# Kernel optimization log

Hardware: AMD Instinct MI355X
Metric: run time of the kernel (lower is better)

Reference implementation:

```python
import jax, jax.numpy as jnp
import numpy as np

B, N, E, H = 1, 4096, 2048, 16
D = E // H  # head_size = 128
DEGREE = 4
LN_EPS = 1e-5
ROPE_BASE = 10000.0


def rope_cos_sin(n, d):
    # [n, d//2] tables
    inv_freq = 1.0 / (ROPE_BASE ** (jnp.arange(0, d, 2, dtype=jnp.float32) / d))
    t = jnp.arange(n, dtype=jnp.float32)[:, None] * inv_freq[None, :]
    return jnp.cos(t), jnp.sin(t)


def apply_rope(x, cos, sin):
    # x: [b, n, h, d]; rotate-half RoPE
    x1, x2 = jnp.split(x, 2, axis=-1)
    c = cos[None, :, None, :]
    s = sin[None, :, None, :]
    return jnp.concatenate([x1 * c - x2 * s, x1 * s + x2 * c], axis=-1)


def layernorm(x, scale, bias, eps=LN_EPS):
    m = jnp.mean(x, axis=-1, keepdims=True)
    v = jnp.var(x, axis=-1, keepdims=True)
    return (x - m) * jax.lax.rsqrt(v + eps) * scale + bias


def polynomial_attention(q, k, v, degree, is_causal):
    # q,k,v: [b, h, n, d]
    a = jnp.einsum('bhnd,bhmd->bhnm', q, k) ** degree
    if is_causal:
        a = jnp.tril(a)
    denom = jnp.sum(a, axis=-1, keepdims=True)
    return jnp.einsum('bhnm,bhmd->bhnd', a / denom, v)


def setup_inputs() -> dict:
    key = jax.random.key(0)
    k0, k1, k2 = jax.random.split(key, 3)
    x = jax.random.normal(k0, (B, N, E), dtype=jnp.float32)
    # Dense(3*emb_dim, use_bias=False) and Dense(emb_dim, use_bias=False)
    w_qkv = jax.random.normal(k1, (E, 3 * E), dtype=jnp.float32) * (1.0 / np.sqrt(E))
    w_out = jax.random.normal(k2, (E, E), dtype=jnp.float32) * (1.0 / np.sqrt(E))
    # shared pre-attention LayerNorm over head dim (flax init: scale=1, bias=0)
    ln_scale = jnp.ones((D,), dtype=jnp.float32)
    ln_bias = jnp.zeros((D,), dtype=jnp.float32)
    return {"x": x, "w_qkv": w_qkv, "w_out": w_out,
            "ln_scale": ln_scale, "ln_bias": ln_bias}


def reference(x, w_qkv, w_out, ln_scale, ln_bias):
    b, n, e = x.shape
    proj = x @ w_qkv                              # [b, n, 3e]
    q, k, v = jnp.split(proj, 3, axis=-1)
    q = q.reshape(b, n, H, D)
    k = k.reshape(b, n, H, D)
    v = v.reshape(b, n, H, D)
    cos, sin = rope_cos_sin(n, D)
    q = apply_rope(q, cos, sin)
    k = apply_rope(k, cos, sin)
    # transpose branch (non-softmax): [b, h, n, d]
    q = q.transpose(0, 2, 1, 3)
    k = k.transpose(0, 2, 1, 3)
    v = v.transpose(0, 2, 1, 3)
    # shared pre_attn LayerNorm applied to q and k
    q = layernorm(q, ln_scale, ln_bias)
    k = layernorm(k, ln_scale, ln_bias)
    out = polynomial_attention(q, k, v, DEGREE, True)  # [b, h, n, d]
    out = out.transpose(0, 2, 1, 3).reshape(b, n, e)
    out = out @ w_out                              # dropout rate 0 / inference: identity
    return out
```

## Files before the change

### kernel.cpp

```cpp
#include <hip/hip_runtime.h>
#include <stdint.h>
#include <math.h>

#define N_SEQ 4096
#define EDIM  2048
#define NH    16
#define HD    128

typedef __attribute__((ext_vector_type(8))) short bf16x8;
typedef __attribute__((ext_vector_type(4))) float f32x4;

#define AS1 __attribute__((address_space(1)))
#define AS3 __attribute__((address_space(3)))

__device__ __forceinline__ void gll16(const unsigned short* g, unsigned short* l) {
    __builtin_amdgcn_global_load_lds((const AS1 unsigned int*)g,
                                     (AS3 unsigned int*)l, 16, 0, 0);
}

__device__ __forceinline__ unsigned short f2bf(float f) {
    union { float f; unsigned u; } v; v.f = f;
    unsigned r = v.u + 0x7FFFu + ((v.u >> 16) & 1u);
    return (unsigned short)(r >> 16);
}
__device__ __forceinline__ float bf2f(unsigned short h) {
    union { unsigned u; float f; } v; v.u = ((unsigned)h) << 16;
    return v.f;
}

__global__ void k_convert_x(const float* __restrict__ x,
                            unsigned short* __restrict__ xb, int n4) {
    int i = blockIdx.x * blockDim.x + threadIdx.x;
    int stride = gridDim.x * blockDim.x;
    for (; i < n4; i += stride) {
        float4 v = ((const float4*)x)[i];
        ushort4 o;
        o.x = f2bf(v.x); o.y = f2bf(v.y); o.z = f2bf(v.z); o.w = f2bf(v.w);
        ((ushort4*)xb)[i] = o;
    }
}

__global__ void k_transpose_f32_bf16(const float* __restrict__ in,
                                     unsigned short* __restrict__ out,
                                     int R, int C) {
    __shared__ unsigned short Ls[64][68];
    const int c0 = blockIdx.x * 64, r0 = blockIdx.y * 64;
    const int t = threadIdx.x;
    #pragma unroll
    for (int i = 0; i < 4; ++i) {
        int ch = i * 256 + t;
        int r = ch >> 4, c4 = (ch & 15) * 4;
        float4 v = *(const float4*)&in[(size_t)(r0 + r) * C + c0 + c4];
        ushort4 o;
        o.x = f2bf(v.x); o.y = f2bf(v.y); o.z = f2bf(v.z); o.w = f2bf(v.w);
        *(ushort4*)&Ls[r][c4] = o;
    }
    __syncthreads();
    #pragma unroll
    for (int i = 0; i < 2; ++i) {
        int ch = i * 256 + t;
        int rr = ch >> 3, c8 = (ch & 7) * 8;
        unsigned short vals[8];
        #pragma unroll
        for (int j = 0; j < 8; ++j) vals[j] = Ls[c8 + j][rr];
        uint4 pk;
        pk.x = (unsigned)vals[0] | ((unsigned)vals[1] << 16);
        pk.y = (unsigned)vals[2] | ((unsigned)vals[3] << 16);
        pk.z = (unsigned)vals[4] | ((unsigned)vals[5] << 16);
        pk.w = (unsigned)vals[6] | ((unsigned)vals[7] << 16);
        *(uint4*)&out[(size_t)(c0 + rr) * R + r0 + c8] = pk;
    }
}

template<int F32OUT>
__launch_bounds__(256, 2)
__global__ void k_gemm_bt(const unsigned short* __restrict__ A,
                          const unsigned short* __restrict__ Bt,
                          void* __restrict__ C,
                          int M, int N, int K) {
    __shared__ unsigned short sh[2 * 128 * 64];
    unsigned short* As = sh;
    unsigned short* Bs = sh + 128 * 64;

    const int t = threadIdx.x;
    const int wave = t >> 6, lane = t & 63;
    const int wm = wave >> 1, wn = wave & 1;
    const int lg = lane >> 4, lr = lane & 15;

    const int nbx = gridDim.x;
    const int nwg = nbx * gridDim.y;
    int bid = blockIdx.y * nbx + blockIdx.x;
    int swz = (bid & 7) * (nwg >> 3) + (bid >> 3);
    const int m0 = (swz / nbx) * 128;
    const int n0 = (swz % nbx) * 128;

    const unsigned short* aptr = A  + (size_t)m0 * K;
    const unsigned short* bptr = Bt + (size_t)n0 * K;

    f32x4 acc[4][4];
    #pragma unroll
    for (int i = 0; i < 4; ++i)
        #pragma unroll
        for (int j = 0; j < 4; ++j) acc[i][j] = f32x4{0.f, 0.f, 0.f, 0.f};

    int schr[4], srow[4], scb[4];
    #pragma unroll
    for (int i = 0; i < 4; ++i) {
        int ch = (i * 4 + wave) * 64 + lane;
        schr[i] = ch;
        srow[i] = ch >> 3;
        scb[i]  = (ch & 7) ^ ((ch >> 3) & 7);
    }

    const int nkb = K >> 6;
    for (int kb = 0; kb < nkb; ++kb) {
        __syncthreads();
        #pragma unroll
        for (int i = 0; i < 4; ++i) {
            const size_t goff = (size_t)srow[i] * K + (size_t)kb * 64 + scb[i] * 8;
            gll16(&aptr[goff], &As[schr[i] * 8]);
            gll16(&bptr[goff], &Bs[schr[i] * 8]);
        }
        __syncthreads();

        #pragma unroll
        for (int kk = 0; kk < 2; ++kk) {
            bf16x8 af[4], bf[4];
            const int cbx = ((kk * 4 + lg) ^ (lr & 7)) * 8;
            #pragma unroll
            for (int i = 0; i < 4; ++i) {
                af[i] = *(const bf16x8*)&As[(wm * 64 + i * 16 + lr) * 64 + cbx];
                bf[i] = *(const bf16x8*)&Bs[(wn * 64 + i * 16 + lr) * 64 + cbx];
            }
            #pragma unroll
            for (int i = 0; i < 4; ++i)
                #pragma unroll
                for (int j = 0; j < 4; ++j)
                    acc[i][j] = __builtin_amdgcn_mfma_f32_16x16x32_bf16(af[i], bf[j], acc[i][j], 0, 0, 0);
        }
    }

    if (F32OUT) {
        #pragma unroll
        for (int i = 0; i < 4; ++i) {
            int row0 = m0 + wm * 64 + i * 16 + lg * 4;
            #pragma unroll
            for (int j = 0; j < 4; ++j) {
                int col = n0 + wn * 64 + j * 16 + lr;
                #pragma unroll
                for (int r = 0; r < 4; ++r)
                    ((float*)C)[(size_t)(row0 + r) * N + col] = acc[i][j][r];
            }
        }
    } else {
        __syncthreads();
        unsigned short* Cs = sh;
        #pragma unroll
        for (int i = 0; i < 4; ++i) {
            #pragma unroll
            for (int j = 0; j < 4; ++j) {
                int col = wn * 64 + j * 16 + lr;
                #pragma unroll
                for (int r = 0; r < 4; ++r)
                    Cs[(wm * 64 + i * 16 + lg * 4 + r) * 128 + col] = f2bf(acc[i][j][r]);
            }
        }
        __syncthreads();
        #pragma unroll
        for (int i = 0; i < 8; ++i) {
            int ch = i * 256 + t;
            int row = ch >> 4, c8 = (ch & 15) * 8;
            *(uint4*)&((unsigned short*)C)[(size_t)(m0 + row) * N + n0 + c8] =
                *(const uint4*)&Cs[row * 128 + c8];
        }
    }
}

__global__ void k_ropeln(const unsigned short* __restrict__ proj,
                         const float* __restrict__ ln_scale,
                         const float* __restrict__ ln_bias,
                         unsigned short* __restrict__ Qh,
                         unsigned short* __restrict__ Kh) {
    const int n = blockIdx.x;
    const int wave = threadIdx.x >> 6, lane = threadIdx.x & 63;
    float inv = expf(-((float)(2 * lane) / 128.0f) * 9.210340371976184f);
    float ang = (float)n * inv;
    float c = cosf(ang), s = sinf(ang);
    const float sc1 = ln_scale[lane], sc2 = ln_scale[lane + 64];
    const float b1 = ln_bias[lane],  b2 = ln_bias[lane + 64];

    for (int r = wave; r < 32; r += 4) {
        int h = r >> 1, qk = r & 1;
        const unsigned short* src = proj + (size_t)n * (3 * EDIM) + qk * EDIM + h * HD;
        float x1 = bf2f(src[lane]), x2 = bf2f(src[lane + 64]);
        float o1 = x1 * c - x2 * s;
        float o2 = x1 * s + x2 * c;
        float sum = o1 + o2, sq = o1 * o1 + o2 * o2;
        #pragma unroll
        for (int d = 1; d < 64; d <<= 1) {
            sum += __shfl_xor(sum, d);
            sq  += __shfl_xor(sq, d);
        }
        float mean = sum * (1.0f / 128.0f);
        float var = sq * (1.0f / 128.0f) - mean * mean;
        float rstd = rsqrtf(var + 1e-5f);
        float y1 = (o1 - mean) * rstd * sc1 + b1;
        float y2 = (o2 - mean) * rstd * sc2 + b2;
        unsigned short* dst = (qk ? Kh : Qh) + ((size_t)h * N_SEQ + n) * HD;
        dst[lane]      = f2bf(y1);
        dst[lane + 64] = f2bf(y2);
    }
}

__global__ void k_vtrans(const unsigned short* __restrict__ proj,
                         unsigned short* __restrict__ Vt) {
    __shared__ unsigned short Ls[64][136];
    const int h = blockIdx.y;
    const int n0 = blockIdx.x * 64;
    const int t = threadIdx.x;
    #pragma unroll
    for (int i = 0; i < 4; ++i) {
        int ch = i * 256 + t;
        int r = ch >> 4, d0 = (ch & 15) * 8;
        uint4 v = *(const uint4*)&proj[(size_t)(n0 + r) * (3 * EDIM) + 2 * EDIM + h * HD + d0];
        *(uint4*)&Ls[r][d0] = v;
    }
    __syncthreads();
    #pragma unroll
    for (int i = 0; i < 4; ++i) {
        int ch = i * 256 + t;
        int d = ch >> 3, p = ch & 7;
        unsigned short vals[8];
        #pragma unroll
        for (int j = 0; j < 8; ++j) {
            int ko = 32 * (p >> 2) + 16 * (j >> 2) + 4 * (p & 3) + (j & 3);
            vals[j] = Ls[ko][d];
        }
        uint4 pk;
        pk.x = (unsigned)vals[0] | ((unsigned)vals[1] << 16);
        pk.y = (unsigned)vals[2] | ((unsigned)vals[3] << 16);
        pk.z = (unsigned)vals[4] | ((unsigned)vals[5] << 16);
        pk.w = (unsigned)vals[6] | ((unsigned)vals[7] << 16);
        *(uint4*)&Vt[((size_t)h * HD + d) * N_SEQ + n0 + p * 8] = pk;
    }
}

__launch_bounds__(256, 2)
__global__ void k_attn(const unsigned short* __restrict__ Qh,
                       const unsigned short* __restrict__ Kh,
                       const unsigned short* __restrict__ Vt,
                       unsigned short* __restrict__ O) {
    __shared__ unsigned short pool[4 * 8192];

    const int t = threadIdx.x;
    const int w = t >> 6, lane = t & 63;
    const int lg = lane >> 4, lr = lane & 15;

    const int s = blockIdx.x & 255;
    const int batch = blockIdx.x >> 8;
    const int x = s & 7;
    const int hb = (s >> 3) & 1;
    const int h = x * 2 + hb;
    const int qq = s >> 4;
    const int qb = batch ? qq : (31 - qq);
    const int q0 = qb * 128;
    const int qbase = q0 + w * 32;

    bf16x8 qf[2][4];
    #pragma unroll
    for (int mi = 0; mi < 2; ++mi)
        #pragma unroll
        for (int kk = 0; kk < 4; ++kk)
            qf[mi][kk] = *(const bf16x8*)&Qh[((size_t)h * N_SEQ + qbase + mi * 16 + lr) * HD + kk * 32 + lg * 8];

    f32x4 acc[2][8];
    #pragma unroll
    for (int i = 0; i < 2; ++i)
        #pragma unroll
        for (int j = 0; j < 8; ++j) acc[i][j] = f32x4{0.f, 0.f, 0.f, 0.f};
    f32x4 accd[2];
    accd[0] = f32x4{0.f, 0.f, 0.f, 0.f};
    accd[1] = f32x4{0.f, 0.f, 0.f, 0.f};

    bf16x8 onesf;
    {
        short ov = (lr == 0) ? (short)0x3F80 : (short)0;
        #pragma unroll
        for (int j = 0; j < 8; ++j) onesf[j] = ov;
    }

    int kch[4], vch[4];
    const unsigned short* kg[4];
    const unsigned short* vg[4];
    #pragma unroll
    for (int i = 0; i < 4; ++i) {
        int ch = i * 256 + t;
        kch[i] = ch;
        int r = ch >> 4, p = ch & 15;
        int csrc = (p & 8) | ((p ^ r) & 7);
        kg[i] = Kh + ((size_t)h * N_SEQ + r) * HD + csrc * 8;
    }
    #pragma unroll
    for (int i = 0; i < 4; ++i) {
        int ch = i * 256 + t;
        vch[i] = ch;
        int d = ch >> 3, p2 = ch & 7;
        int c2src = (p2 ^ d) & 7;
        vg[i] = Vt + ((size_t)h * HD + d) * N_SEQ + c2src * 8;
    }

    const int nkb = 2 * qb + 2;

    union U8 { unsigned u[4]; bf16x8 v; };

    auto stage = [&](unsigned short* Kn, unsigned short* Vn) {
        #pragma unroll
        for (int i = 0; i < 4; ++i) { gll16(kg[i], Kn + kch[i] * 8); kg[i] += 64 * HD; }
        #pragma unroll
        for (int i = 0; i < 4; ++i) { gll16(vg[i], Vn + vch[i] * 8); vg[i] += 64; }
    };

    auto compute = [&](int k0, const unsigned short* Kc, const unsigned short* Vc) {
        f32x4 sa[2][4];
        #pragma unroll
        for (int i = 0; i < 2; ++i)
            #pragma unroll
            for (int j = 0; j < 4; ++j) sa[i][j] = f32x4{0.f, 0.f, 0.f, 0.f};
        #pragma unroll
        for (int nn = 0; nn < 2; ++nn) {
            bf16x8 kf[2][4];
            #pragma unroll
            for (int nj = 0; nj < 2; ++nj)
                #pragma unroll
                for (int kk = 0; kk < 4; ++kk) {
                    int row = (nn * 2 + nj) * 16 + lr;
                    int c = kk * 4 + lg;
                    int cs = (c & 8) | ((c ^ row) & 7);
                    kf[nj][kk] = *(const bf16x8*)&Kc[row * 128 + cs * 8];
                }
            __builtin_amdgcn_s_setprio(1);
            #pragma unroll
            for (int kk = 0; kk < 4; ++kk)
                #pragma unroll
                for (int nj = 0; nj < 2; ++nj)
                    #pragma unroll
                    for (int mi = 0; mi < 2; ++mi)
                        sa[mi][nn * 2 + nj] = __builtin_amdgcn_mfma_f32_16x16x32_bf16(
                            kf[nj][kk], qf[mi][kk], sa[mi][nn * 2 + nj], 0, 0, 0);
            __builtin_amdgcn_s_setprio(0);
        }

        unsigned wreg[2][4][2];
        const bool nomask = (k0 + 63 <= qbase);
        #pragma unroll
        for (int mi = 0; mi < 2; ++mi)
            #pragma unroll
            for (int nj = 0; nj < 4; ++nj) {
                float p[4];
                #pragma unroll
                for (int r = 0; r < 4; ++r) {
                    float sv = sa[mi][nj][r];
                    float t2 = sv * sv;
                    p[r] = t2 * t2;
                    if (!nomask) {
                        int gk = k0 + nj * 16 + lg * 4 + r;
                        int gq = qbase + mi * 16 + lr;
                        p[r] = (gk <= gq) ? p[r] : 0.0f;
                    }
                }
                asm("v_cvt_pk_bf16_f32 %0, %1, %2" : "=v"(wreg[mi][nj][0]) : "v"(p[0]), "v"(p[1]));
                asm("v_cvt_pk_bf16_f32 %0, %1, %2" : "=v"(wreg[mi][nj][1]) : "v"(p[2]), "v"(p[3]));
            }

        #pragma unroll
        for (int s2 = 0; s2 < 2; ++s2) {
            bf16x8 pa[2];
            #pragma unroll
            for (int mi = 0; mi < 2; ++mi) {
                U8 u;
                u.u[0] = wreg[mi][2 * s2][0];
                u.u[1] = wreg[mi][2 * s2][1];
                u.u[2] = wreg[mi][2 * s2 + 1][0];
                u.u[3] = wreg[mi][2 * s2 + 1][1];
                pa[mi] = u.v;
            }
            __builtin_amdgcn_s_setprio(1);
            #pragma unroll
            for (int ni = 0; ni < 8; ++ni) {
                int d = ni * 16 + lr;
                int cs = ((s2 * 4 + lg) ^ (d & 7)) & 7;
                bf16x8 vf = *(const bf16x8*)&Vc[d * 64 + cs * 8];
                #pragma unroll
                for (int mi = 0; mi < 2; ++mi)
                    acc[mi][ni] = __builtin_amdgcn_mfma_f32_16x16x32_bf16(pa[mi], vf, acc[mi][ni], 0, 0, 0);
            }
            #pragma unroll
            for (int mi = 0; mi < 2; ++mi)
                accd[mi] = __builtin_amdgcn_mfma_f32_16x16x32_bf16(pa[mi], onesf, accd[mi], 0, 0, 0);
            __builtin_amdgcn_s_setprio(0);
        }
    };

    stage(pool, pool + 16384);

    for (int kb = 0; kb < nkb; kb += 2) {
        stage(pool + 8192, pool + 16384 + 8192);
        asm volatile("s_waitcnt vmcnt(8)" ::: "memory");
        __builtin_amdgcn_s_barrier();
        compute(kb * 64, pool, pool + 16384);
        __builtin_amdgcn_s_barrier();
        if (kb + 2 < nkb) {
            stage(pool, pool + 16384);
            asm volatile("s_waitcnt vmcnt(8)" ::: "memory");
        } else {
            asm volatile("s_waitcnt vmcnt(0)" ::: "memory");
        }
        __builtin_amdgcn_s_barrier();
        compute((kb + 1) * 64, pool + 8192, pool + 16384 + 8192);
        __builtin_amdgcn_s_barrier();
    }

    unsigned short* Cs = pool;
    #pragma unroll
    for (int mi = 0; mi < 2; ++mi) {
        #pragma unroll
        for (int r = 0; r < 4; ++r) {
            float dv = __shfl(accd[mi][r], lane & 48);
            float rinv = 1.0f / dv;
            int rw = w * 32 + mi * 16 + lg * 4 + r;
            #pragma unroll
            for (int ni = 0; ni < 8; ++ni)
                Cs[rw * 128 + ni * 16 + lr] = f2bf(acc[mi][ni][r] * rinv);
        }
    }
    __syncthreads();
    #pragma unroll
    for (int i = 0; i < 8; ++i) {
        int ch = i * 256 + t;
        int row = ch >> 4, c8 = (ch & 15) * 8;
        *(uint4*)&O[(size_t)(q0 + row) * EDIM + h * HD + c8] = *(const uint4*)&Cs[row * 128 + c8];
    }
}

extern "C" void kernel_launch(void* const* d_in, const int* in_sizes, int n_in,
                              void* d_out, int out_size, void* d_ws, size_t ws_size,
                              hipStream_t stream) {
    const float* x        = (const float*)d_in[0];
    const float* w_qkv    = (const float*)d_in[1];
    const float* w_out    = (const float*)d_in[2];
    const float* ln_scale = (const float*)d_in[3];
    const float* ln_bias  = (const float*)d_in[4];

    if (ws_size < 134217728u) return;

    char* ws = (char*)d_ws;
    unsigned short* xb    = (unsigned short*)(ws);
    unsigned short* wqkvT = (unsigned short*)(ws + 16777216);
    unsigned short* woutT = (unsigned short*)(ws + 41943040);
    unsigned short* proj  = (unsigned short*)(ws + 50331648);
    unsigned short* Kh    = (unsigned short*)(ws + 100663296);
    unsigned short* Vt    = (unsigned short*)(ws + 117440512);
    unsigned short* Qh    = wqkvT;
    unsigned short* attnO = xb;

    k_convert_x<<<2048, 256, 0, stream>>>(x, xb, (N_SEQ * EDIM) / 4);
    k_transpose_f32_bf16<<<dim3(3 * EDIM / 64, EDIM / 64), 256, 0, stream>>>(w_qkv, wqkvT, EDIM, 3 * EDIM);
    k_transpose_f32_bf16<<<dim3(EDIM / 64, EDIM / 64), 256, 0, stream>>>(w_out, woutT, EDIM, EDIM);
    k_gemm_bt<0><<<dim3(3 * EDIM / 128, N_SEQ / 128), 256, 0, stream>>>(xb, wqkvT, proj, N_SEQ, 3 * EDIM, EDIM);
    k_ropeln<<<N_SEQ, 256, 0, stream>>>(proj, ln_scale, ln_bias, Qh, Kh);
    k_vtrans<<<dim3(N_SEQ / 64, NH), 256, 0, stream>>>(proj, Vt);
    k_attn<<<512, 256, 0, stream>>>(Qh, Kh, Vt, attnO);
    k_gemm_bt<1><<<dim3(EDIM / 128, N_SEQ / 128), 256, 0, stream>>>(attnO, woutT, (float*)d_out, N_SEQ, EDIM, EDIM);
}
```

Baseline: 305.4 us.

## Split attention key range across warps with 64-row query tiles and LDS reduction

Each attention block now covers 64 query rows instead of 128, and the grid doubles to 1024 blocks. The four warps form a 2x2 grid: two split the queries and two split each 64-key tile, each taking 32 keys. The two key halves' partial output and denominator accumulators are summed through LDS before normalising. Warps whose key half lies fully above the causal diagonal skip their work, and an odd tile count gets a single-tile prologue. The aim is more blocks and better load balance across CUs. The cost is K/V staged once per 64 queries, doubling K/V traffic, plus an extra LDS reduction with more barriers.

```diff
diff --git a/kernel.cpp b/kernel.cpp
--- a/kernel.cpp
+++ b/kernel.cpp
@@ -254,17 +254,15 @@
 
     const int t = threadIdx.x;
     const int w = t >> 6, lane = t & 63;
+    const int wq = w >> 1, wk = w & 1;
     const int lg = lane >> 4, lr = lane & 15;
 
-    const int s = blockIdx.x & 255;
-    const int batch = blockIdx.x >> 8;
-    const int x = s & 7;
-    const int hb = (s >> 3) & 1;
-    const int h = x * 2 + hb;
-    const int qq = s >> 4;
-    const int qb = batch ? qq : (31 - qq);
-    const int q0 = qb * 128;
-    const int qbase = q0 + w * 32;
+    const int b = blockIdx.x;
+    const int h = (b & 7) * 2 + ((b >> 3) & 1);
+    const int qt = 63 - (b >> 4);
+    const int q0 = qt * 64;
+    const int qbase = q0 + wq * 32;
+    const int kbase = wk * 32;
 
     bf16x8 qf[2][4];
     #pragma unroll
@@ -309,7 +307,7 @@
         vg[i] = Vt + ((size_t)h * HD + d) * N_SEQ + c2src * 8;
     }
 
-    const int nkb = 2 * qb + 2;
+    const int nkb = qt + 1;
 
     union U8 { unsigned u[4]; bf16x8 v; };
 
@@ -321,41 +319,40 @@
     };
 
     auto compute = [&](int k0, const unsigned short* Kc, const unsigned short* Vc) {
-        f32x4 sa[2][4];
-        #pragma unroll
-        for (int i = 0; i < 2; ++i)
-            #pragma unroll
-            for (int j = 0; j < 4; ++j) sa[i][j] = f32x4{0.f, 0.f, 0.f, 0.f};
-        #pragma unroll
-        for (int nn = 0; nn < 2; ++nn) {
-            bf16x8 kf[2][4];
+        if (k0 + kbase > qbase + 31) return;
+        f32x4 sa[2][2];
+        #pragma unroll
+        for (int i = 0; i < 2; ++i) {
+            sa[i][0] = f32x4{0.f, 0.f, 0.f, 0.f};
+            sa[i][1] = f32x4{0.f, 0.f, 0.f, 0.f};
+        }
+        bf16x8 kf[2][4];
+        #pragma unroll
+        for (int nj = 0; nj < 2; ++nj)
+            #pragma unroll
+            for (int kk = 0; kk < 4; ++kk) {
+                int row = kbase + nj * 16 + lr;
+                int c = kk * 4 + lg;
+                int cs = (c & 8) | ((c ^ row) & 7);
+                kf[nj][kk] = *(const bf16x8*)&Kc[row * 128 + cs * 8];
+            }
+        __builtin_amdgcn_s_setprio(1);
+        #pragma unroll
+        for (int kk = 0; kk < 4; ++kk)
             #pragma unroll
             for (int nj = 0; nj < 2; ++nj)
                 #pragma unroll
-                for (int kk = 0; kk < 4; ++kk) {
-                    int row = (nn * 2 + nj) * 16 + lr;
-                    int c = kk * 4 + lg;
-                    int cs = (c & 8) | ((c ^ row) & 7);
-                    kf[nj][kk] = *(const bf16x8*)&Kc[row * 128 + cs * 8];
-                }
-            __builtin_amdgcn_s_setprio(1);
-            #pragma unroll
-            for (int kk = 0; kk < 4; ++kk)
-                #pragma unroll
-                for (int nj = 0; nj < 2; ++nj)
-                    #pragma unroll
-                    for (int mi = 0; mi < 2; ++mi)
-                        sa[mi][nn * 2 + nj] = __builtin_amdgcn_mfma_f32_16x16x32_bf16(
-                            kf[nj][kk], qf[mi][kk], sa[mi][nn * 2 + nj], 0, 0, 0);
-            __builtin_amdgcn_s_setprio(0);
-        }
-
-        unsigned wreg[2][4][2];
-        const bool nomask = (k0 + 63 <= qbase);
+                for (int mi = 0; mi < 2; ++mi)
+                    sa[mi][nj] = __builtin_amdgcn_mfma_f32_16x16x32_bf16(
+                        kf[nj][kk], qf[mi][kk], sa[mi][nj], 0, 0, 0);
+        __builtin_amdgcn_s_setprio(0);
+
+        unsigned wreg[2][2][2];
+        const bool nomask = (k0 + kbase + 31 <= qbase);
         #pragma unroll
         for (int mi = 0; mi < 2; ++mi)
             #pragma unroll
-            for (int nj = 0; nj < 4; ++nj) {
+            for (int nj = 0; nj < 2; ++nj) {
                 float p[4];
                 #pragma unroll
                 for (int r = 0; r < 4; ++r) {
@@ -363,7 +360,7 @@
                     float t2 = sv * sv;
                     p[r] = t2 * t2;
                     if (!nomask) {
-                        int gk = k0 + nj * 16 + lg * 4 + r;
+                        int gk = k0 + kbase + nj * 16 + lg * 4 + r;
                         int gq = qbase + mi * 16 + lr;
                         p[r] = (gk <= gq) ? p[r] : 0.0f;
                     }
@@ -372,38 +369,43 @@
                 asm("v_cvt_pk_bf16_f32 %0, %1, %2" : "=v"(wreg[mi][nj][1]) : "v"(p[2]), "v"(p[3]));
             }
 
-        #pragma unroll
-        for (int s2 = 0; s2 < 2; ++s2) {
-            bf16x8 pa[2];
-            #pragma unroll
-            for (int mi = 0; mi < 2; ++mi) {
-                U8 u;
-                u.u[0] = wreg[mi][2 * s2][0];
-                u.u[1] = wreg[mi][2 * s2][1];
-                u.u[2] = wreg[mi][2 * s2 + 1][0];
-                u.u[3] = wreg[mi][2 * s2 + 1][1];
-                pa[mi] = u.v;
-            }
-            __builtin_amdgcn_s_setprio(1);
-            #pragma unroll
-            for (int ni = 0; ni < 8; ++ni) {
-                int d = ni * 16 + lr;
-                int cs = ((s2 * 4 + lg) ^ (d & 7)) & 7;
-                bf16x8 vf = *(const bf16x8*)&Vc[d * 64 + cs * 8];
-                #pragma unroll
-                for (int mi = 0; mi < 2; ++mi)
-                    acc[mi][ni] = __builtin_amdgcn_mfma_f32_16x16x32_bf16(pa[mi], vf, acc[mi][ni], 0, 0, 0);
-            }
+        bf16x8 pa[2];
+        #pragma unroll
+        for (int mi = 0; mi < 2; ++mi) {
+            U8 u;
+            u.u[0] = wreg[mi][0][0];
+            u.u[1] = wreg[mi][0][1];
+            u.u[2] = wreg[mi][1][0];
+            u.u[3] = wreg[mi][1][1];
+            pa[mi] = u.v;
+        }
+        __builtin_amdgcn_s_setprio(1);
+        #pragma unroll
+        for (int ni = 0; ni < 8; ++ni) {
+            int d = ni * 16 + lr;
+            int cs = ((wk * 4 + lg) ^ (d & 7)) & 7;
+            bf16x8 vf = *(const bf16x8*)&Vc[d * 64 + cs * 8];
             #pragma unroll
             for (int mi = 0; mi < 2; ++mi)
-                accd[mi] = __builtin_amdgcn_mfma_f32_16x16x32_bf16(pa[mi], onesf, accd[mi], 0, 0, 0);
-            __builtin_amdgcn_s_setprio(0);
-        }
+                acc[mi][ni] = __builtin_amdgcn_mfma_f32_16x16x32_bf16(pa[mi], vf, acc[mi][ni], 0, 0, 0);
+        }
+        #pragma unroll
+        for (int mi = 0; mi < 2; ++mi)
+            accd[mi] = __builtin_amdgcn_mfma_f32_16x16x32_bf16(pa[mi], onesf, accd[mi], 0, 0, 0);
+        __builtin_amdgcn_s_setprio(0);
     };
 
     stage(pool, pool + 16384);
-
-    for (int kb = 0; kb < nkb; kb += 2) {
+    int kb0 = 0;
+    if (nkb & 1) {
+        asm volatile("s_waitcnt vmcnt(0)" ::: "memory");
+        __builtin_amdgcn_s_barrier();
+        compute(0, pool, pool + 16384);
+        __builtin_amdgcn_s_barrier();
+        if (nkb > 1) stage(pool, pool + 16384);
+        kb0 = 1;
+    }
+    for (int kb = kb0; kb < nkb; kb += 2) {
         stage(pool + 8192, pool + 16384 + 8192);
         asm volatile("s_waitcnt vmcnt(8)" ::: "memory");
         __builtin_amdgcn_s_barrier();
@@ -420,22 +422,50 @@
         __builtin_amdgcn_s_barrier();
     }
 
-    unsigned short* Cs = pool;
-    #pragma unroll
-    for (int mi = 0; mi < 2; ++mi) {
-        #pragma unroll
-        for (int r = 0; r < 4; ++r) {
-            float dv = __shfl(accd[mi][r], lane & 48);
-            float rinv = 1.0f / dv;
-            int rw = w * 32 + mi * 16 + lg * 4 + r;
+    asm volatile("s_waitcnt vmcnt(0)" ::: "memory");
+    __syncthreads();
+    float* Xf = (float*)pool;
+    const int xbase = wq * 4608 + lane * 4;
+    if (wk == 1) {
+        #pragma unroll
+        for (int mi = 0; mi < 2; ++mi) {
             #pragma unroll
             for (int ni = 0; ni < 8; ++ni)
-                Cs[rw * 128 + ni * 16 + lr] = f2bf(acc[mi][ni][r] * rinv);
+                *(f32x4*)&Xf[xbase + (mi * 8 + ni) * 256] = acc[mi][ni];
+            *(f32x4*)&Xf[xbase + (16 + mi) * 256] = accd[mi];
         }
     }
     __syncthreads();
-    #pragma unroll
-    for (int i = 0; i < 8; ++i) {
+    unsigned short* Cs = pool + 20480;
+    if (wk == 0) {
+        #pragma unroll
+        for (int mi = 0; mi < 2; ++mi) {
+            #pragma unroll
+            for (int ni = 0; ni < 8; ++ni) {
+                f32x4 o = *(const f32x4*)&Xf[xbase + (mi * 8 + ni) * 256];
+                acc[mi][ni][0] += o[0]; acc[mi][ni][1] += o[1];
+                acc[mi][ni][2] += o[2]; acc[mi][ni][3] += o[3];
+            }
+            f32x4 od = *(const f32x4*)&Xf[xbase + (16 + mi) * 256];
+            accd[mi][0] += od[0]; accd[mi][1] += od[1];
+            accd[mi][2] += od[2]; accd[mi][3] += od[3];
+        }
+        #pragma unroll
+        for (int mi = 0; mi < 2; ++mi) {
+            #pragma unroll
+            for (int r = 0; r < 4; ++r) {
+                float dv = __shfl(accd[mi][r], lane & 48);
+                float rinv = 1.0f / dv;
+                int rw = wq * 32 + mi * 16 + lg * 4 + r;
+                #pragma unroll
+                for (int ni = 0; ni < 8; ++ni)
+                    Cs[rw * 128 + ni * 16 + lr] = f2bf(acc[mi][ni][r] * rinv);
+            }
+        }
+    }
+    __syncthreads();
+    #pragma unroll
+    for (int i = 0; i < 4; ++i) {
         int ch = i * 256 + t;
         int row = ch >> 4, c8 = (ch & 15) * 8;
         *(uint4*)&O[(size_t)(q0 + row) * EDIM + h * HD + c8] = *(const uint4*)&Cs[row * 128 + c8];
@@ -469,6 +499,6 @@
     k_gemm_bt<0><<<dim3(3 * EDIM / 128, N_SEQ / 128), 256, 0, stream>>>(xb, wqkvT, proj, N_SEQ, 3 * EDIM, EDIM);
     k_ropeln<<<N_SEQ, 256, 0, stream>>>(proj, ln_scale, ln_bias, Qh, Kh);
     k_vtrans<<<dim3(N_SEQ / 64, NH), 256, 0, stream>>>(proj, Vt);
-    k_attn<<<512, 256, 0, stream>>>(Qh, Kh, Vt, attnO);
+    k_attn<<<1024, 256, 0, stream>>>(Qh, Kh, Vt, attnO);
     k_gemm_bt<1><<<dim3(EDIM / 128, N_SEQ / 128), 256, 0, stream>>>(attnO, woutT, (float*)d_out, N_SEQ, EDIM, EDIM);
 }
```

Result: faster. 286.3 us (-6.2%).
